# Optimization experiments

Hardware: AMD Instinct MI355X
Metric: run time of the kernel (lower is better)

Reference implementation:

```python
import jax, jax.numpy as jnp
import numpy as np

BL = 512  # block length (self.bl)

def _conv1x1(x, W, b):
    # x: [B, Cin, L], W: [Cout, Cin], b: [Cout]
    return jnp.einsum('bcl,oc->bol', x, W) + b[None, :, None]


def setup_inputs() -> dict:
    key = jax.random.key(0)
    ks = jax.random.split(key, 10)
    B, L = 4, 8192
    q_dim = k_dim = v_dim = 512
    c = q_dim // 2  # r1=r2=r3=2 -> 256
    s = 0.05
    return {
        'x1': jax.random.normal(ks[0], (B, q_dim, L), jnp.float32),
        'mask': jnp.ones((B, 1, L), jnp.float32),
        'Wq': jax.random.normal(ks[1], (c, q_dim), jnp.float32) * s,
        'bq': jnp.zeros((c,), jnp.float32),
        'Wk': jax.random.normal(ks[2], (c, k_dim), jnp.float32) * s,
        'bk': jnp.zeros((c,), jnp.float32),
        'Wv': jax.random.normal(ks[3], (c, v_dim), jnp.float32) * s,
        'bv': jnp.zeros((c,), jnp.float32),
        'Wo': jax.random.normal(ks[4], (v_dim, c), jnp.float32) * s,
        'bo': jnp.zeros((v_dim,), jnp.float32),
    }


def _sliding_att(q, k, v, mask):
    B, c1, L = q.shape
    c3 = v.shape[1]
    nb = L // BL
    half = BL // 2
    ws = BL + 2 * half  # window size
    # queries per block: [B*nb, c1, BL]
    qb = q.reshape(B, c1, nb, BL).transpose(0, 2, 1, 3).reshape(B * nb, c1, BL)
    # overlapping k/v/mask windows via gather (unfold equivalent)
    idx = jnp.arange(nb)[:, None] * BL + jnp.arange(ws)[None, :]  # [nb, ws]
    def windows(t, C):
        tp = jnp.pad(t, ((0, 0), (0, 0), (half, half)))
        tw = tp[:, :, idx]                       # [B, C, nb, ws]
        return tw.transpose(0, 2, 1, 3).reshape(B * nb, C, ws)
    kb = windows(k, c1)
    vb = windows(v, c3)
    mb = windows(mask, 1)                        # [B*nb, 1, ws]
    energy = jnp.einsum('mcq,mck->mqk', qb, kb) / jnp.sqrt(jnp.float32(c1))
    energy = energy + jnp.log(mb + 1e-6)         # mb broadcasts over q dim
    att = jax.nn.softmax(energy, axis=-1) * mb   # [B*nb, BL, ws]
    out = jnp.einsum('mck,mqk->mcq', vb, att)    # [B*nb, c3, BL]
    return out, nb


def reference(x1, mask, Wq, bq, Wk, bk, Wv, bv, Wo, bo):
    q = _conv1x1(x1, Wq, bq)
    k = _conv1x1(x1, Wk, bk)
    v = _conv1x1(x1, Wv, bv)   # encoder: value from x1
    B, _, L = q.shape
    out, nb = _sliding_att(q, k, v, mask)
    out = _conv1x1(jax.nn.relu(out), Wo, bo)     # [B*nb, v_dim, BL]
    v_dim = Wo.shape[0]
    out = out.reshape(B, nb, v_dim, BL).transpose(0, 2, 1, 3).reshape(B, v_dim, L)
    return out * mask[:, 0:1, :]
```

## Files before the change

kernel.cpp:

```cpp
#include <hip/hip_runtime.h>

typedef short short8 __attribute__((ext_vector_type(8)));
typedef float f32x4 __attribute__((ext_vector_type(4)));
typedef unsigned short ushort4v __attribute__((ext_vector_type(4)));

#define MFMA(a, b, c) __builtin_amdgcn_mfma_f32_16x16x32_bf16((a), (b), (c), 0, 0, 0)

__device__ __forceinline__ short f2bf(float f) {
  union { float f; unsigned u; } v; v.f = f;
  unsigned r = v.u + 0x7fffu + ((v.u >> 16) & 1u);
  return (short)(r >> 16);
}

__device__ __forceinline__ void glds16(const short* g, short* l) {
  __builtin_amdgcn_global_load_lds((const __attribute__((address_space(1))) void*)g,
                                   (__attribute__((address_space(3))) void*)l, 16, 0, 0);
}

__global__ __launch_bounds__(256) void convert_w(
    const float* __restrict__ Wq, const float* __restrict__ Wk,
    const float* __restrict__ Wv, const float* __restrict__ Wo,
    const float* __restrict__ bq, const float* __restrict__ bk,
    const float* __restrict__ bv,
    short* __restrict__ Wb3, short* __restrict__ Wob, float* __restrict__ b3) {
  int idx = blockIdx.x * 256 + threadIdx.x;
  const int NW3 = 768 * 512, NWO = 512 * 256;
  if (idx < NW3) {
    int o = idx >> 9, cix = idx & 511;
    const float* W = (o < 256) ? Wq : (o < 512) ? Wk : Wv;
    Wb3[idx] = f2bf(W[(o & 255) * 512 + cix]);
  } else if (idx < NW3 + NWO) {
    int i2 = idx - NW3;
    Wob[i2] = f2bf(Wo[i2]);
  } else if (idx < NW3 + NWO + 768) {
    int i3 = idx - (NW3 + NWO);
    b3[i3] = (i3 < 256) ? bq[i3] : (i3 < 512) ? bk[i3 - 256] : bv[i3 - 512];
  }
}

__global__ __launch_bounds__(256) void transpose_x(const float* __restrict__ x,
                                                   short* __restrict__ xT) {
  __shared__ float t[64][65];
  int b = blockIdx.z, c0 = blockIdx.y * 64, l0 = blockIdx.x * 64;
  int tid = threadIdx.x;
  {
    int cl = tid >> 2, ls = (tid & 3) * 16;
    const float* xb = x + ((size_t)b * 512 + c0 + cl) * 8192 + l0 + ls;
#pragma unroll
    for (int i = 0; i < 4; i++) {
      f32x4 v = *(const f32x4*)(xb + i * 4);
      *(f32x4*)&t[cl][ls + i * 4] = v;
    }
  }
  __syncthreads();
  {
    int ll = tid >> 2, cs = (tid & 3) * 16;
    short8 pk[2];
#pragma unroll
    for (int h = 0; h < 2; h++)
#pragma unroll
      for (int j = 0; j < 8; j++) pk[h][j] = f2bf(t[cs + h * 8 + j][ll]);
    short* xo = xT + ((size_t)b * 8192 + l0 + ll) * 512 + c0 + cs;
    *(short8*)(xo) = pk[0];
    *(short8*)(xo + 8) = pk[1];
  }
}

__global__ __launch_bounds__(256, 2) void gemm_qkv(
    const short* __restrict__ Wb3, const float* __restrict__ b3,
    const short* __restrict__ xT, short* __restrict__ q_t,
    short* __restrict__ k_t, short* __restrict__ v_tt) {
  __shared__ __align__(16) short lds[16384];
  int t = threadIdx.x, w = t >> 6, l = t & 63;
  int r = l & 15, g = l >> 4;
  int wr = w >> 1, wc = w & 1;
  int id = blockIdx.x;
  int xcd = id & 7, j = id >> 3;
  int grp = j / 6, mtile = j - 6 * grp;
  int g_total = xcd * 32 + grp;
  int n0 = (g_total >> 2) * 128, b = g_total & 3;
  int m00 = mtile * 128;
  const short* Ab = Wb3 + (size_t)m00 * 512;
  const short* Bb = xT + (size_t)b * 8192 * 512 + (size_t)n0 * 512;
  int c0 = w * 64 + l, c1 = 256 + w * 64 + l;
  int a0r = c0 >> 2, a0c = (c0 & 3) * 8, a1r = c1 >> 2, a1c = (c1 & 3) * 8;

  auto STAGE = [&](int buf, int kk) {
    const short* ga = Ab + kk * 32;
    const short* gb = Bb + kk * 32;
    short* lb = lds + buf * 8192;
    glds16(ga + (size_t)a0r * 512 + a0c, lb + (w * 64) * 8);
    glds16(ga + (size_t)a1r * 512 + a1c, lb + (256 + w * 64) * 8);
    glds16(gb + (size_t)a0r * 512 + a0c, lb + 4096 + (w * 64) * 8);
    glds16(gb + (size_t)a1r * 512 + a1c, lb + 4096 + (256 + w * 64) * 8);
  };

  f32x4 acc[4][4];
#pragma unroll
  for (int i = 0; i < 4; i++)
#pragma unroll
    for (int jj = 0; jj < 4; jj++) acc[i][jj] = {0.f, 0.f, 0.f, 0.f};

  STAGE(0, 0);
  __syncthreads();
  int cur = 0;
  for (int kk = 0; kk < 16; kk++) {
    if (kk + 1 < 16) STAGE(cur ^ 1, kk + 1);
    const short* lb = lds + cur * 8192;
    short8 af[4], bfv[4];
#pragma unroll
    for (int mt = 0; mt < 4; mt++)
      af[mt] = *(const short8*)(lb + (wr * 64 + mt * 16 + r) * 32 + g * 8);
#pragma unroll
    for (int nt = 0; nt < 4; nt++)
      bfv[nt] = *(const short8*)(lb + 4096 + (wc * 64 + nt * 16 + r) * 32 + g * 8);
#pragma unroll
    for (int mt = 0; mt < 4; mt++)
#pragma unroll
      for (int nt = 0; nt < 4; nt++) acc[mt][nt] = MFMA(af[mt], bfv[nt], acc[mt][nt]);
    __syncthreads();
    cur ^= 1;
  }

  if (mtile < 4) {
    short* dst = ((mtile < 2) ? q_t : k_t) + (size_t)b * 8192 * 256;
    int cb = (mtile & 1) * 128 + wr * 64;
#pragma unroll
    for (int nt = 0; nt < 4; nt++) {
      int n = n0 + wc * 64 + nt * 16 + r;
#pragma unroll
      for (int mt = 0; mt < 4; mt++) {
        ushort4v pk;
#pragma unroll
        for (int jj = 0; jj < 4; jj++)
          pk[jj] = (unsigned short)f2bf(acc[mt][nt][jj] + b3[m00 + wr * 64 + mt * 16 + 4 * g + jj]);
        *(ushort4v*)(dst + (size_t)n * 256 + cb + mt * 16 + 4 * g) = pk;
      }
    }
  } else {
    short* dst = v_tt + (size_t)b * 256 * 8192;
    int cb = (mtile - 4) * 128 + wr * 64;
#pragma unroll
    for (int mt = 0; mt < 4; mt++)
#pragma unroll
      for (int jj = 0; jj < 4; jj++) {
        int c = cb + mt * 16 + 4 * g + jj;
        float bias = b3[512 + c];
#pragma unroll
        for (int nt = 0; nt < 4; nt++)
          dst[(size_t)c * 8192 + n0 + wc * 64 + nt * 16 + r] = f2bf(acc[mt][nt][jj] + bias);
      }
  }
}

__global__ __launch_bounds__(256, 2) void attn(
    const short* __restrict__ q_t, const short* __restrict__ k_t,
    const short* __restrict__ v_tt, const float* __restrict__ mask,
    short* __restrict__ attout) {
  __shared__ __align__(16) short kv[37376];
  int t = threadIdx.x;
  int lane = t & 63, w = t >> 6;
  int r = lane & 15, g = lane >> 4;
  int id = blockIdx.x;
  int xcd = id & 7, m8 = id >> 3;
  int qtile = m8 & 7;
  int grp = ((m8 >> 3) << 3) + xcd;
  int blk = grp & 15, b = grp >> 4;
  const short* qtb = q_t + (size_t)b * 8192 * 256;
  const short* ktb = k_t + (size_t)b * 8192 * 256;
  const short* vtb = v_tt + (size_t)b * 256 * 8192;
  const float* mrow = mask + (size_t)b * 8192;
  int q0 = blk * 512 + qtile * 64 + w * 16;
  short* plds_w = kv + 32768 + w * 1152;

  short8 qf[8];
#pragma unroll
  for (int cc = 0; cc < 8; cc++)
    qf[cc] = *(const short8*)(qtb + (size_t)(q0 + r) * 256 + cc * 32 + g * 8);

  f32x4 zero = {0.f, 0.f, 0.f, 0.f};
  short8 zero8 = {0, 0, 0, 0, 0, 0, 0, 0};
  f32x4 o[16];
#pragma unroll
  for (int i = 0; i < 16; i++) o[i] = zero;
  float m_run[4] = {-1e30f, -1e30f, -1e30f, -1e30f};
  float lsum[4] = {0.f, 0.f, 0.f, 0.f};
  int wbase = blk * 512 - 256;

  short8 kreg[8], vreg[8];
  float mreg[4];
  auto ld_chunk = [&](int kbase) {
#pragma unroll
    for (int i = 0; i < 8; i++) {
      int s = t + i * 256;
      int row = s >> 5, sl = s & 31;
      int kg = kbase + row;
      kreg[i] = zero8;
      if (kg >= 0 && kg < 8192) kreg[i] = *(const short8*)(ktb + (size_t)kg * 256 + sl * 8);
    }
#pragma unroll
    for (int i = 0; i < 8; i++) {
      int s = t + i * 256;
      int chn = s >> 3, sl = s & 7;
      int kg = kbase + sl * 8;
      vreg[i] = zero8;
      if (kg >= 0 && kg <= 8192 - 8) vreg[i] = *(const short8*)(vtb + (size_t)chn * 8192 + kg);
    }
#pragma unroll
    for (int kt = 0; kt < 4; kt++) {
      int kg = kbase + kt * 16 + r;
      mreg[kt] = (kg >= 0 && kg < 8192) ? mrow[kg] : 0.f;
    }
  };
  auto st_chunk = [&]() {
#pragma unroll
    for (int i = 0; i < 8; i++) {
      int s = t + i * 256;
      int row = s >> 5, sl = s & 31;
      *(short8*)(kv + row * 256 + ((sl ^ (row & 7)) * 8)) = kreg[i];
    }
#pragma unroll
    for (int i = 0; i < 8; i++) {
      int s = t + i * 256;
      int chn = s >> 3, sl = s & 7;
      *(short8*)(kv + 16384 + chn * 64 + ((sl ^ (chn & 7)) * 8)) = vreg[i];
    }
  };

  ld_chunk(wbase);

  for (int ch = 0; ch < 16; ch++) {
    int kbase = wbase + ch * 64;
    float mvv[4];
#pragma unroll
    for (int kt = 0; kt < 4; kt++) mvv[kt] = mreg[kt];
    st_chunk();
    asm volatile("s_waitcnt lgkmcnt(0)" ::: "memory");
    __builtin_amdgcn_s_barrier();
    if (ch < 15) ld_chunk(kbase + 64);
    __builtin_amdgcn_sched_barrier(0);

    f32x4 e[4];
    float lm[4];
#pragma unroll
    for (int kt = 0; kt < 4; kt++) {
      e[kt] = zero;
      lm[kt] = __logf(mvv[kt] + 1e-6f);
      const short* kr = kv + (kt * 16 + r) * 256;
#pragma unroll
      for (int cc = 0; cc < 8; cc++) {
        short8 kf = *(const short8*)(kr + (((cc * 4 + g) ^ (r & 7)) * 8));
        e[kt] = MFMA(qf[cc], kf, e[kt]);
      }
    }
#pragma unroll
    for (int kt = 0; kt < 4; kt++)
#pragma unroll
      for (int j = 0; j < 4; j++) e[kt][j] = e[kt][j] * 0.0625f + lm[kt];
    float mx[4];
#pragma unroll
    for (int j = 0; j < 4; j++)
      mx[j] = fmaxf(fmaxf(e[0][j], e[1][j]), fmaxf(e[2][j], e[3][j]));
#pragma unroll
    for (int d = 1; d < 16; d <<= 1)
#pragma unroll
      for (int j = 0; j < 4; j++) mx[j] = fmaxf(mx[j], __shfl_xor(mx[j], d));
    float need = 0.f;
#pragma unroll
    for (int j = 0; j < 4; j++) need = fmaxf(need, mx[j] - m_run[j]);
    if (!__all(need <= 8.f)) {
      float scl[4];
#pragma unroll
      for (int j = 0; j < 4; j++) {
        float mn = fmaxf(m_run[j], mx[j]);
        scl[j] = __expf(m_run[j] - mn);
        m_run[j] = mn;
        lsum[j] *= scl[j];
      }
#pragma unroll
      for (int ct = 0; ct < 16; ct++)
#pragma unroll
        for (int j = 0; j < 4; j++) o[ct][j] *= scl[j];
    }
#pragma unroll
    for (int kt = 0; kt < 4; kt++)
#pragma unroll
      for (int j = 0; j < 4; j++) {
        float p = __expf(e[kt][j] - m_run[j]);
        lsum[j] += p;
        e[kt][j] = p * mvv[kt];
      }

#pragma unroll
    for (int kt = 0; kt < 4; kt++)
#pragma unroll
      for (int j = 0; j < 4; j++)
        plds_w[(4 * g + j) * 72 + kt * 16 + r] = f2bf(e[kt][j]);

#pragma unroll
    for (int ks = 0; ks < 2; ks++) {
      short8 pa = *(const short8*)(plds_w + r * 72 + ks * 32 + g * 8);
#pragma unroll
      for (int ct = 0; ct < 16; ct++) {
        short8 vf = *(const short8*)(kv + 16384 + (ct * 16 + r) * 64 +
                                     (((ks * 4 + g) ^ (r & 7)) * 8));
        o[ct] = MFMA(pa, vf, o[ct]);
      }
    }
    if (ch < 15) {
      asm volatile("s_waitcnt lgkmcnt(0)" ::: "memory");
      __builtin_amdgcn_s_barrier();
    }
  }
#pragma unroll
  for (int d = 1; d < 16; d <<= 1)
#pragma unroll
    for (int j = 0; j < 4; j++) lsum[j] += __shfl_xor(lsum[j], d);
  float inv[4];
#pragma unroll
  for (int j = 0; j < 4; j++) inv[j] = 1.0f / lsum[j];
  short* ao = attout + (size_t)b * 8192 * 256;
#pragma unroll
  for (int ct = 0; ct < 16; ct++)
#pragma unroll
    for (int j = 0; j < 4; j++) {
      float vv = fmaxf(o[ct][j] * inv[j], 0.f);
      ao[(size_t)(q0 + 4 * g + j) * 256 + ct * 16 + r] = f2bf(vv);
    }
}

__global__ __launch_bounds__(256, 2) void gemm_out(
    const short* __restrict__ Wob, const float* __restrict__ bo,
    const short* __restrict__ attout, const float* __restrict__ mask,
    float* __restrict__ out) {
  __shared__ __align__(16) short lds[16384];
  int t = threadIdx.x, w = t >> 6, l = t & 63;
  int r = l & 15, g = l >> 4;
  int wr = w >> 1, wc = w & 1;
  int id = blockIdx.x;
  int xcd = id & 7, j = id >> 3;
  int grp = j >> 2, member = j & 3;
  int g_total = xcd * 32 + grp;
  int n0 = (g_total >> 2) * 128, b = g_total & 3;
  int m00 = member * 128;
  const short* Ab = Wob + (size_t)m00 * 256;
  const short* Bb = attout + (size_t)b * 8192 * 256 + (size_t)n0 * 256;
  int c0 = w * 64 + l, c1 = 256 + w * 64 + l;
  int a0r = c0 >> 2, a0c = (c0 & 3) * 8, a1r = c1 >> 2, a1c = (c1 & 3) * 8;

  auto STAGE = [&](int buf, int kk) {
    const short* ga = Ab + kk * 32;
    const short* gb = Bb + kk * 32;
    short* lb = lds + buf * 8192;
    glds16(ga + (size_t)a0r * 256 + a0c, lb + (w * 64) * 8);
    glds16(ga + (size_t)a1r * 256 + a1c, lb + (256 + w * 64) * 8);
    glds16(gb + (size_t)a0r * 256 + a0c, lb + 4096 + (w * 64) * 8);
    glds16(gb + (size_t)a1r * 256 + a1c, lb + 4096 + (256 + w * 64) * 8);
  };

  f32x4 acc[4][4];
#pragma unroll
  for (int i = 0; i < 4; i++)
#pragma unroll
    for (int jj = 0; jj < 4; jj++) acc[i][jj] = {0.f, 0.f, 0.f, 0.f};

  STAGE(0, 0);
  __syncthreads();
  int cur = 0;
  for (int kk = 0; kk < 8; kk++) {
    if (kk + 1 < 8) STAGE(cur ^ 1, kk + 1);
    const short* lb = lds + cur * 8192;
    short8 af[4], bfv[4];
#pragma unroll
    for (int mt = 0; mt < 4; mt++)
      af[mt] = *(const short8*)(lb + (wr * 64 + mt * 16 + r) * 32 + g * 8);
#pragma unroll
    for (int nt = 0; nt < 4; nt++)
      bfv[nt] = *(const short8*)(lb + 4096 + (wc * 64 + nt * 16 + r) * 32 + g * 8);
#pragma unroll
    for (int mt = 0; mt < 4; mt++)
#pragma unroll
      for (int nt = 0; nt < 4; nt++) acc[mt][nt] = MFMA(af[mt], bfv[nt], acc[mt][nt]);
    __syncthreads();
    cur ^= 1;
  }

  float* ob = out + (size_t)b * 512 * 8192;
#pragma unroll
  for (int nt = 0; nt < 4; nt++) {
    int n = n0 + wc * 64 + nt * 16 + r;
    float mv = mask[(size_t)b * 8192 + n];
#pragma unroll
    for (int mt = 0; mt < 4; mt++)
#pragma unroll
      for (int jj = 0; jj < 4; jj++) {
        int m = m00 + wr * 64 + mt * 16 + 4 * g + jj;
        ob[(size_t)m * 8192 + n] = (acc[mt][nt][jj] + bo[m]) * mv;
      }
  }
}

extern "C" void kernel_launch(void* const* d_in, const int* in_sizes, int n_in,
                              void* d_out, int out_size, void* d_ws, size_t ws_size,
                              hipStream_t stream) {
  const float* x1 = (const float*)d_in[0];
  const float* mask = (const float*)d_in[1];
  const float* Wq = (const float*)d_in[2];
  const float* bq = (const float*)d_in[3];
  const float* Wk = (const float*)d_in[4];
  const float* bk = (const float*)d_in[5];
  const float* Wv = (const float*)d_in[6];
  const float* bv = (const float*)d_in[7];
  const float* Wo = (const float*)d_in[8];
  const float* bo = (const float*)d_in[9];

  char* ws = (char*)d_ws;
  size_t off = 0;
  short* xT = (short*)(ws + off);  off += (size_t)4 * 8192 * 512 * 2;
  short* q_t = (short*)(ws + off); off += (size_t)4 * 8192 * 256 * 2;
  short* k_t = (short*)(ws + off); off += (size_t)4 * 8192 * 256 * 2;
  short* v_tt = (short*)(ws + off); off += (size_t)4 * 8192 * 256 * 2;
  short* aout = (short*)(ws + off); off += (size_t)4 * 8192 * 256 * 2;
  short* Wb3 = (short*)(ws + off); off += 768 * 512 * 2;
  short* Wob = (short*)(ws + off); off += 512 * 256 * 2;
  float* b3 = (float*)(ws + off);  off += 768 * 4;

  convert_w<<<dim3(2051), dim3(256), 0, stream>>>(Wq, Wk, Wv, Wo, bq, bk, bv, Wb3, Wob, b3);
  transpose_x<<<dim3(128, 8, 4), dim3(256), 0, stream>>>(x1, xT);
  gemm_qkv<<<dim3(1536), dim3(256), 0, stream>>>(Wb3, b3, xT, q_t, k_t, v_tt);
  attn<<<dim3(512), dim3(256), 0, stream>>>(q_t, k_t, v_tt, mask, aout);
  gemm_out<<<dim3(1024), dim3(256), 0, stream>>>(Wob, bo, aout, mask, (float*)d_out);
}
```

Before: 311.8 us.

## Read K and V fragments directly from global memory instead of staging in LDS

Removes the shared-memory K/V staging (register prefetch, swizzled LDS stores and block barriers) and has each wave load its MFMA operands for K and V straight from global memory, with clamped addresses for out-of-range keys. LDS shrinks to the per-wave P buffer, which could allow more resident blocks. The cost is that each of the four waves now issues its own redundant global loads for the shared K/V chunk, relying on cache hits. The loads are also no longer prefetched ahead of compute, so memory latency is exposed inside the loop.

```diff
diff --git a/kernel.cpp b/kernel.cpp
--- a/kernel.cpp
+++ b/kernel.cpp
@@ -157,7 +157,7 @@
     const short* __restrict__ q_t, const short* __restrict__ k_t,
     const short* __restrict__ v_tt, const float* __restrict__ mask,
     short* __restrict__ attout) {
-  __shared__ __align__(16) short kv[37376];
+  __shared__ __align__(16) short plds[4][16][72];
   int t = threadIdx.x;
   int lane = t & 63, w = t >> 6;
   int r = lane & 15, g = lane >> 4;
@@ -171,7 +171,7 @@
   const short* vtb = v_tt + (size_t)b * 256 * 8192;
   const float* mrow = mask + (size_t)b * 8192;
   int q0 = blk * 512 + qtile * 64 + w * 16;
-  short* plds_w = kv + 32768 + w * 1152;
+  short (*pw)[72] = plds[w];
 
   short8 qf[8];
 #pragma unroll
@@ -179,7 +179,6 @@
     qf[cc] = *(const short8*)(qtb + (size_t)(q0 + r) * 256 + cc * 32 + g * 8);
 
   f32x4 zero = {0.f, 0.f, 0.f, 0.f};
-  short8 zero8 = {0, 0, 0, 0, 0, 0, 0, 0};
   f32x4 o[16];
 #pragma unroll
   for (int i = 0; i < 16; i++) o[i] = zero;
@@ -187,69 +186,23 @@
   float lsum[4] = {0.f, 0.f, 0.f, 0.f};
   int wbase = blk * 512 - 256;
 
-  short8 kreg[8], vreg[8];
-  float mreg[4];
-  auto ld_chunk = [&](int kbase) {
-#pragma unroll
-    for (int i = 0; i < 8; i++) {
-      int s = t + i * 256;
-      int row = s >> 5, sl = s & 31;
-      int kg = kbase + row;
-      kreg[i] = zero8;
-      if (kg >= 0 && kg < 8192) kreg[i] = *(const short8*)(ktb + (size_t)kg * 256 + sl * 8);
-    }
-#pragma unroll
-    for (int i = 0; i < 8; i++) {
-      int s = t + i * 256;
-      int chn = s >> 3, sl = s & 7;
-      int kg = kbase + sl * 8;
-      vreg[i] = zero8;
-      if (kg >= 0 && kg <= 8192 - 8) vreg[i] = *(const short8*)(vtb + (size_t)chn * 8192 + kg);
-    }
-#pragma unroll
-    for (int kt = 0; kt < 4; kt++) {
-      int kg = kbase + kt * 16 + r;
-      mreg[kt] = (kg >= 0 && kg < 8192) ? mrow[kg] : 0.f;
-    }
-  };
-  auto st_chunk = [&]() {
-#pragma unroll
-    for (int i = 0; i < 8; i++) {
-      int s = t + i * 256;
-      int row = s >> 5, sl = s & 31;
-      *(short8*)(kv + row * 256 + ((sl ^ (row & 7)) * 8)) = kreg[i];
-    }
-#pragma unroll
-    for (int i = 0; i < 8; i++) {
-      int s = t + i * 256;
-      int chn = s >> 3, sl = s & 7;
-      *(short8*)(kv + 16384 + chn * 64 + ((sl ^ (chn & 7)) * 8)) = vreg[i];
-    }
-  };
-
-  ld_chunk(wbase);
-
   for (int ch = 0; ch < 16; ch++) {
     int kbase = wbase + ch * 64;
-    float mvv[4];
-#pragma unroll
-    for (int kt = 0; kt < 4; kt++) mvv[kt] = mreg[kt];
-    st_chunk();
-    asm volatile("s_waitcnt lgkmcnt(0)" ::: "memory");
-    __builtin_amdgcn_s_barrier();
-    if (ch < 15) ld_chunk(kbase + 64);
-    __builtin_amdgcn_sched_barrier(0);
-
     f32x4 e[4];
-    float lm[4];
+    float lm[4], mvv[4];
 #pragma unroll
     for (int kt = 0; kt < 4; kt++) {
       e[kt] = zero;
-      lm[kt] = __logf(mvv[kt] + 1e-6f);
-      const short* kr = kv + (kt * 16 + r) * 256;
+      int kg = kbase + kt * 16 + r;
+      bool val = (kg >= 0) && (kg < 8192);
+      int kgc = val ? kg : (kg < 0 ? 0 : 8191);
+      float mv = val ? mrow[kg] : 0.f;
+      mvv[kt] = mv;
+      lm[kt] = __logf(mv + 1e-6f);
+      const short* kr = ktb + (size_t)kgc * 256;
 #pragma unroll
       for (int cc = 0; cc < 8; cc++) {
-        short8 kf = *(const short8*)(kr + (((cc * 4 + g) ^ (r & 7)) * 8));
+        short8 kf = *(const short8*)(kr + cc * 32 + g * 8);
         e[kt] = MFMA(qf[cc], kf, e[kt]);
       }
     }
@@ -295,21 +248,18 @@
     for (int kt = 0; kt < 4; kt++)
 #pragma unroll
       for (int j = 0; j < 4; j++)
-        plds_w[(4 * g + j) * 72 + kt * 16 + r] = f2bf(e[kt][j]);
+        pw[4 * g + j][kt * 16 + r] = f2bf(e[kt][j]);
 
 #pragma unroll
     for (int ks = 0; ks < 2; ks++) {
-      short8 pa = *(const short8*)(plds_w + r * 72 + ks * 32 + g * 8);
+      short8 pa = *(const short8*)&pw[r][ks * 32 + g * 8];
+      int kg0 = kbase + ks * 32 + g * 8;
+      int kgc0 = min(max(kg0, 0), 8192 - 8);
 #pragma unroll
       for (int ct = 0; ct < 16; ct++) {
-        short8 vf = *(const short8*)(kv + 16384 + (ct * 16 + r) * 64 +
-                                     (((ks * 4 + g) ^ (r & 7)) * 8));
+        short8 vf = *(const short8*)(vtb + (size_t)(ct * 16 + r) * 8192 + kgc0);
         o[ct] = MFMA(pa, vf, o[ct]);
       }
-    }
-    if (ch < 15) {
-      asm volatile("s_waitcnt lgkmcnt(0)" ::: "memory");
-      __builtin_amdgcn_s_barrier();
     }
   }
 #pragma unroll
```

New measurement: 436.2 us. +39.9%, slower.
